# Kernel optimization log

Measured on AMD Instinct MI355X. Metric: run time of the kernel, lower is better.

## Reference

```python
import jax, jax.numpy as jnp
import numpy as np

EPS = 1e-5
SLOPE = 0.1


def _leaky(v):
    return jnp.where(v >= 0, v, SLOPE * v)


def _bn(v, gamma, beta):
    # v: (C, Q, k); training-mode batch norm over (Q, k) with biased variance
    m = v.mean(axis=(1, 2), keepdims=True)
    var = v.var(axis=(1, 2), keepdims=True)
    return (v - m) * jax.lax.rsqrt(var + EPS) * gamma[:, None, None] + beta[:, None, None]


def setup_inputs() -> dict:
    key = jax.random.key(0)
    ks = jax.random.split(key, 6)
    Q, S, K, F, O = 16384, 16384, 32, 64, 64
    q_points = jax.random.normal(ks[0], (Q, 3), dtype=jnp.float32)
    s_points = jax.random.normal(ks[1], (S, 3), dtype=jnp.float32)
    neighb_inds = jax.random.randint(ks[2], (Q, K), 0, S + 1)  # S is the padded zero row
    feat = jax.random.normal(ks[3], (S, F), dtype=jnp.float32)
    conv0_w = jax.random.normal(ks[4], (O, F), dtype=jnp.float32) * 0.1
    conv1_w = jax.random.normal(ks[5], (O * 3, O), dtype=jnp.float32) * 0.1
    return {
        "q_points": q_points,
        "s_points": s_points,
        "feat": feat,
        "neighb_inds": neighb_inds,
        "conv0_w": conv0_w,
        "gamma0": jnp.ones((O,), jnp.float32),
        "beta0": jnp.zeros((O,), jnp.float32),
        "conv1_w": conv1_w,
        "gamma1": jnp.ones((O,), jnp.float32),
        "beta1": jnp.zeros((O,), jnp.float32),
    }


def reference(q_points, s_points, feat, neighb_inds, conv0_w, gamma0, beta0, conv1_w, gamma1, beta1):
    Q, K = neighb_inds.shape
    n_supports = s_points.shape[0]
    out_c = conv1_w.shape[1]
    in_c = conv1_w.shape[0] // out_c  # = 3 for feat_mode='xyz'

    # pad with a zero row (index n_supports is the 'out of range' shadow point)
    s_pad = jnp.concatenate([s_points, jnp.zeros((1, s_points.shape[1]), s_points.dtype)], 0)
    f_pad = jnp.concatenate([feat, jnp.zeros((1, feat.shape[1]), feat.dtype)], 0)

    # relative xyz feature; zero out shadow neighbors
    x = s_pad[neighb_inds] - q_points[:, None, :]          # (Q, K, 3)
    mask = (neighb_inds == n_supports)[..., None]
    x = jnp.where(mask, jnp.zeros((), x.dtype), x)

    y = f_pad[neighb_inds]                                  # (Q, K, F)

    # kernel generation: conv0 (1x1) -> BN -> LeakyReLU -> conv1 (1x1)
    h = jnp.einsum('of,qkf->oqk', conv0_w, y)               # (O, Q, K)
    h = _leaky(_bn(h, gamma0, beta0))
    ker = jnp.einsum('co,oqk->qkc', conv1_w, h)             # (Q, K, O*in_c)
    ker = ker.reshape(Q, K, out_c, in_c)                    # (Q, K, O, 3)

    # per-edge matmul against relative xyz, then BN -> LeakyReLU -> max over k
    z = jnp.einsum('qkoi,qki->oqk', ker, x)                 # (O, Q, K)
    z = _leaky(_bn(z, gamma1, beta1))
    z = z.max(axis=2)                                       # (O, Q)
    return z.T                                              # (Q, O)
```

## Files before the change

### kernel.cpp

```cpp
#include <hip/hip_runtime.h>
#include <hip/hip_bf16.h>

typedef __attribute__((ext_vector_type(8))) short bf16x8;
typedef __attribute__((ext_vector_type(4))) short bf16x4;
typedef __attribute__((ext_vector_type(4))) float f32x4;

#define LEAKY(v) ((v) >= 0.f ? (v) : 0.1f * (v))

constexpr int Q = 16384, S = 16384, KNN = 32, F = 64, O = 64;
constexpr int NEDGE = Q * KNN;
constexpr int QB = 8;
constexpr int EB = 256;
constexpr int GD = Q / QB;
constexpr int GH = 128;
constexpr int FP = 72;
constexpr float EPSV = 1e-5f;

constexpr size_t CNT_OFF  = 0;
constexpr size_t P0_OFF   = 65536;
constexpr size_t ST0_OFF  = P0_OFF + (size_t)GH * 128 * 4;
constexpr size_t ZMIN_OFF = ST0_OFF + 512;
constexpr size_t P1_OFF   = ZMIN_OFF + (size_t)Q * O * 4;
constexpr size_t ST1_OFF  = P1_OFF + (size_t)GD * 128 * 4;
constexpr size_t W0F_OFF  = ST1_OFF + 512;
constexpr size_t W1F_OFF  = W0F_OFF + 8192;

__device__ __forceinline__ short f2bf(float f) {
  __hip_bfloat16 h = __float2bfloat16(f);
  short r; __builtin_memcpy(&r, &h, 2); return r;
}

__global__ void k_hist(const int* __restrict__ inds, int* __restrict__ cnt) {
  int i = blockIdx.x * blockDim.x + threadIdx.x;
  int stride = gridDim.x * blockDim.x;
  for (; i < NEDGE; i += stride) {
    int idx = inds[i];
    if (idx < S) atomicAdd(&cnt[idx], 1);
  }
}

__global__ void k_prep(const float* __restrict__ w0g, const float* __restrict__ w1g,
                       short* __restrict__ w0f, short* __restrict__ w1f) {
  const int t = blockIdx.x * 256 + threadIdx.x;
  const int fa = t >> 6, ln = t & 63;
  const int l4 = ln >> 4, l15 = ln & 15;
  if (fa < 8) {
    const int mt = fa >> 1, kk = fa & 1;
    const int o = 16 * mt + l15, f = 32 * kk + 8 * l4;
    const float* src = w0g + o * 64 + f;
    bf16x8 pk;
#pragma unroll
    for (int j = 0; j < 8; ++j) pk[j] = f2bf(src[j]);
    *(bf16x8*)&w0f[t * 8] = pk;
  } else {
    const int fb = fa - 8;
    const int nt = fb >> 1, kk = fb & 1;
    const int i = nt >> 2, b = nt & 3;
    const int o = 16 * b + l15, op = 32 * kk + 8 * l4;
    const float* src = w1g + (o * 3 + i) * 64 + op;
    bf16x8 pk;
#pragma unroll
    for (int j = 0; j < 8; ++j) pk[j] = f2bf(src[j]);
    *(bf16x8*)&w1f[(fb * 64 + ln) * 8] = pk;
  }
}

__global__ void k_hsq(const float* __restrict__ feat, const int* __restrict__ cnt,
                      const short* __restrict__ w0f, float* __restrict__ p0) {
  __shared__ float sred[4][2][64];
  const int t = threadIdx.x, blk = blockIdx.x;
  const int wv = t >> 6, ln = t & 63, l4 = ln >> 4, l15 = ln & 15;

  const bf16x8* w0v = (const bf16x8*)w0f;
  bf16x8 w0a[8];
#pragma unroll
  for (int fa = 0; fa < 8; ++fa) w0a[fa] = w0v[fa * 64 + ln];

  float hs[4][4], hq[4][4];
#pragma unroll
  for (int mt = 0; mt < 4; ++mt)
#pragma unroll
    for (int r = 0; r < 4; ++r) { hs[mt][r] = 0.f; hq[mt][r] = 0.f; }

#pragma unroll
  for (int tile = 0; tile < 2; ++tile) {
    const int s0 = blk * 128 + (wv * 2 + tile) * 16;
    const float wc = (float)cnt[s0 + l15];
    const float4* fr = (const float4*)(feat + (size_t)(s0 + l15) * 64);
    float4 a = fr[2 * l4], b = fr[2 * l4 + 1];
    float4 c = fr[8 + 2 * l4], d = fr[9 + 2 * l4];
    bf16x8 y0, y1;
    y0[0] = f2bf(a.x); y0[1] = f2bf(a.y); y0[2] = f2bf(a.z); y0[3] = f2bf(a.w);
    y0[4] = f2bf(b.x); y0[5] = f2bf(b.y); y0[6] = f2bf(b.z); y0[7] = f2bf(b.w);
    y1[0] = f2bf(c.x); y1[1] = f2bf(c.y); y1[2] = f2bf(c.z); y1[3] = f2bf(c.w);
    y1[4] = f2bf(d.x); y1[5] = f2bf(d.y); y1[6] = f2bf(d.z); y1[7] = f2bf(d.w);
#pragma unroll
    for (int mt = 0; mt < 4; ++mt) {
      f32x4 acc = {0.f, 0.f, 0.f, 0.f};
      acc = __builtin_amdgcn_mfma_f32_16x16x32_bf16(w0a[2 * mt], y0, acc, 0, 0, 0);
      acc = __builtin_amdgcn_mfma_f32_16x16x32_bf16(w0a[2 * mt + 1], y1, acc, 0, 0, 0);
#pragma unroll
      for (int r = 0; r < 4; ++r) {
        float h = acc[r];
        hs[mt][r] += wc * h;
        hq[mt][r] += wc * h * h;
      }
    }
  }
#pragma unroll
  for (int mt = 0; mt < 4; ++mt)
#pragma unroll
    for (int r = 0; r < 4; ++r) {
      float s = hs[mt][r], q = hq[mt][r];
#pragma unroll
      for (int d = 1; d < 16; d <<= 1) { s += __shfl_xor(s, d); q += __shfl_xor(q, d); }
      hs[mt][r] = s; hq[mt][r] = q;
    }
  if (l15 == 0) {
#pragma unroll
    for (int mt = 0; mt < 4; ++mt)
#pragma unroll
      for (int r = 0; r < 4; ++r) {
        const int o = 16 * mt + 4 * l4 + r;
        sred[wv][0][o] = hs[mt][r];
        sred[wv][1][o] = hq[mt][r];
      }
  }
  __syncthreads();
  if (t < 128) {
    const int qq = t >> 6, o = t & 63;
    p0[(size_t)blk * 128 + t] =
        sred[0][qq][o] + sred[1][qq][o] + sred[2][qq][o] + sred[3][qq][o];
  }
}

__global__ void k_stats0(const float* __restrict__ p0, const float* __restrict__ g0,
                         const float* __restrict__ b0, float* __restrict__ st0) {
  const int t = threadIdx.x;
  if (t < O) {
    float s = 0.f, q = 0.f;
    for (int b = 0; b < GH; ++b) {
      s += p0[(size_t)b * 128 + t];
      q += p0[(size_t)b * 128 + 64 + t];
    }
    const float invN = 1.f / (float)NEDGE;
    float mean = s * invN;
    float var = q * invN - mean * mean;
    float sc = g0[t] * rsqrtf(var + EPSV);
    st0[t] = sc;
    st0[O + t] = b0[t] - mean * sc;
  }
}

__launch_bounds__(256, 3)
__global__ void k_main(const float* __restrict__ qpts, const float* __restrict__ spts,
                       const float* __restrict__ feat, const int* __restrict__ inds,
                       const short* __restrict__ w0f, const short* __restrict__ w1f,
                       const float* __restrict__ st0,
                       float* __restrict__ zmax, float* __restrict__ zmin,
                       float* __restrict__ p1) {
  __shared__ __align__(16) short ybuf[EB * FP];
  __shared__ __align__(16) float xb[3 * EB];
  __shared__ float swred[4][128];

  const int t = threadIdx.x, blk = blockIdx.x;
  const int wv = t >> 6, ln = t & 63, l4 = ln >> 4, l15 = ln & 15;

  {
    const int e = t;
    const int idx = inds[(size_t)blk * EB + e];
    const int q = blk * QB + (e >> 5);
    float x0 = 0.f, x1 = 0.f, x2 = 0.f;
    if (idx < S) {
      x0 = spts[idx * 3 + 0] - qpts[q * 3 + 0];
      x1 = spts[idx * 3 + 1] - qpts[q * 3 + 1];
      x2 = spts[idx * 3 + 2] - qpts[q * 3 + 2];
      const float4* fr = (const float4*)(feat + (size_t)idx * F);
#pragma unroll
      for (int c = 0; c < 8; ++c) {
        float4 a = fr[2 * c], b = fr[2 * c + 1];
        bf16x8 pk;
        pk[0] = f2bf(a.x); pk[1] = f2bf(a.y); pk[2] = f2bf(a.z); pk[3] = f2bf(a.w);
        pk[4] = f2bf(b.x); pk[5] = f2bf(b.y); pk[6] = f2bf(b.z); pk[7] = f2bf(b.w);
        *(bf16x8*)&ybuf[e * FP + 8 * c] = pk;
      }
    } else {
      bf16x8 pk;
#pragma unroll
      for (int j = 0; j < 8; ++j) pk[j] = 0;
#pragma unroll
      for (int c = 0; c < 8; ++c) *(bf16x8*)&ybuf[e * FP + 8 * c] = pk;
    }
    xb[0 * EB + e] = x0; xb[1 * EB + e] = x1; xb[2 * EB + e] = x2;
  }

  float scr[4][4], shr[4][4];
#pragma unroll
  for (int mt = 0; mt < 4; ++mt)
#pragma unroll
    for (int r = 0; r < 4; ++r) {
      int o = 16 * mt + 4 * l4 + r;
      scr[mt][r] = st0[o]; shr[mt][r] = st0[O + o];
    }

  const bf16x8* w0v = (const bf16x8*)w0f;
  bf16x8 w0a[8];
#pragma unroll
  for (int fa = 0; fa < 8; ++fa) w0a[fa] = w0v[fa * 64 + ln];

  __syncthreads();

#pragma unroll
  for (int nt = 0; nt < 4; ++nt) {
    const int erow = wv * 64 + nt * 16 + l15;
    bf16x8 y0 = *(const bf16x8*)&ybuf[erow * FP + 8 * l4];
    bf16x8 y1 = *(const bf16x8*)&ybuf[erow * FP + 32 + 8 * l4];
#pragma unroll
    for (int mt = 0; mt < 4; ++mt) {
      f32x4 acc = {0.f, 0.f, 0.f, 0.f};
      acc = __builtin_amdgcn_mfma_f32_16x16x32_bf16(w0a[2 * mt], y0, acc, 0, 0, 0);
      acc = __builtin_amdgcn_mfma_f32_16x16x32_bf16(w0a[2 * mt + 1], y1, acc, 0, 0, 0);
      bf16x4 hv;
#pragma unroll
      for (int r = 0; r < 4; ++r) {
        float v = acc[r] * scr[mt][r] + shr[mt][r];
        v = LEAKY(v);
        hv[r] = f2bf(v);
      }
      *(bf16x4*)&ybuf[erow * FP + 16 * mt + 4 * l4] = hv;
    }
  }

  bf16x8 hA[4][2];
  f32x4 xv[4][3];
#pragma unroll
  for (int mt = 0; mt < 4; ++mt) {
    const int erow = wv * 64 + mt * 16 + l15;
    hA[mt][0] = *(const bf16x8*)&ybuf[erow * FP + 8 * l4];
    hA[mt][1] = *(const bf16x8*)&ybuf[erow * FP + 32 + 8 * l4];
    const int ex = wv * 64 + mt * 16 + 4 * l4;
#pragma unroll
    for (int i = 0; i < 3; ++i) xv[mt][i] = *(const f32x4*)&xb[i * EB + ex];
  }

  const bf16x8* w1v = (const bf16x8*)w1f;
  float zmx[2][4], zmn[2][4], zs[4], zq[4];
#pragma unroll
  for (int j = 0; j < 4; ++j) {
    zs[j] = 0.f; zq[j] = 0.f;
    zmx[0][j] = -3.4e38f; zmx[1][j] = -3.4e38f;
    zmn[0][j] = 3.4e38f;  zmn[1][j] = 3.4e38f;
  }

#pragma unroll
  for (int b = 0; b < 4; ++b) {
    bf16x8 w1b[6];
#pragma unroll
    for (int i = 0; i < 3; ++i)
#pragma unroll
      for (int kk = 0; kk < 2; ++kk)
        w1b[i * 2 + kk] = w1v[(((i * 4 + b) * 2) + kk) * 64 + ln];
#pragma unroll
    for (int mt = 0; mt < 4; ++mt) {
      f32x4 z4 = {0.f, 0.f, 0.f, 0.f};
#pragma unroll
      for (int i = 0; i < 3; ++i) {
        f32x4 acc = {0.f, 0.f, 0.f, 0.f};
        acc = __builtin_amdgcn_mfma_f32_16x16x32_bf16(hA[mt][0], w1b[2 * i], acc, 0, 0, 0);
        acc = __builtin_amdgcn_mfma_f32_16x16x32_bf16(hA[mt][1], w1b[2 * i + 1], acc, 0, 0, 0);
#pragma unroll
        for (int r = 0; r < 4; ++r) z4[r] += acc[r] * xv[mt][i][r];
      }
      const int qh = mt >> 1;
#pragma unroll
      for (int r = 0; r < 4; ++r) {
        float v = z4[r];
        zmx[qh][b] = fmaxf(zmx[qh][b], v);
        zmn[qh][b] = fminf(zmn[qh][b], v);
        zs[b] += v; zq[b] += v * v;
      }
    }
  }

#pragma unroll
  for (int qh = 0; qh < 2; ++qh)
#pragma unroll
    for (int b = 0; b < 4; ++b) {
      float m = zmx[qh][b];
      m = fmaxf(m, __shfl_xor(m, 16)); m = fmaxf(m, __shfl_xor(m, 32));
      zmx[qh][b] = m;
      float n = zmn[qh][b];
      n = fminf(n, __shfl_xor(n, 16)); n = fminf(n, __shfl_xor(n, 32));
      zmn[qh][b] = n;
    }
#pragma unroll
  for (int b = 0; b < 4; ++b) {
    float s = zs[b];  s += __shfl_xor(s, 16);  s += __shfl_xor(s, 32);  zs[b] = s;
    float sq = zq[b]; sq += __shfl_xor(sq, 16); sq += __shfl_xor(sq, 32); zq[b] = sq;
  }

  if (l4 == 0) {
#pragma unroll
    for (int qh = 0; qh < 2; ++qh) {
      const int q = blk * QB + wv * 2 + qh;
#pragma unroll
      for (int b = 0; b < 4; ++b) {
        zmax[(size_t)q * O + 16 * b + l15] = zmx[qh][b];
        zmin[(size_t)q * O + 16 * b + l15] = zmn[qh][b];
      }
    }
#pragma unroll
    for (int b = 0; b < 4; ++b) {
      swred[wv][16 * b + l15] = zs[b];
      swred[wv][64 + 16 * b + l15] = zq[b];
    }
  }
  __syncthreads();
  if (t < 128)
    p1[(size_t)blk * 128 + t] = swred[0][t] + swred[1][t] + swred[2][t] + swred[3][t];
}

__global__ void k_red1(const float* __restrict__ p1, const float* __restrict__ g1,
                       const float* __restrict__ b1, float* __restrict__ st1) {
  __shared__ float rs[256], rq[256];
  const int o = blockIdx.x, t = threadIdx.x;
  float s = 0.f, q = 0.f;
  for (int r = t; r < GD; r += 256) {
    s += p1[(size_t)r * 128 + o];
    q += p1[(size_t)r * 128 + 64 + o];
  }
  rs[t] = s; rq[t] = q;
  __syncthreads();
  for (int off = 128; off > 0; off >>= 1) {
    if (t < off) { rs[t] += rs[t + off]; rq[t] += rq[t + off]; }
    __syncthreads();
  }
  if (t == 0) {
    const float invN = 1.f / (float)NEDGE;
    float mean = rs[0] * invN;
    float var = rq[0] * invN - mean * mean;
    float sc = g1[o] * rsqrtf(var + EPSV);
    st1[o] = sc;
    st1[O + o] = b1[o] - mean * sc;
  }
}

__global__ void k_final(const float* __restrict__ st1, const float* __restrict__ zmin,
                        float* __restrict__ out) {
  int i = blockIdx.x * blockDim.x + threadIdx.x;
  if (i < Q * O) {
    int o = i & 63;
    float sc = st1[o], sh = st1[O + o];
    float base = (sc >= 0.f) ? out[i] : zmin[i];
    float v = base * sc + sh;
    out[i] = LEAKY(v);
  }
}

extern "C" void kernel_launch(void* const* d_in, const int* in_sizes, int n_in,
                              void* d_out, int out_size, void* d_ws, size_t ws_size,
                              hipStream_t stream) {
  const float* qpts = (const float*)d_in[0];
  const float* spts = (const float*)d_in[1];
  const float* feat = (const float*)d_in[2];
  const int*   inds = (const int*)d_in[3];
  const float* w0   = (const float*)d_in[4];
  const float* g0   = (const float*)d_in[5];
  const float* b0   = (const float*)d_in[6];
  const float* w1   = (const float*)d_in[7];
  const float* g1   = (const float*)d_in[8];
  const float* b1   = (const float*)d_in[9];
  float* out = (float*)d_out;

  char* ws = (char*)d_ws;
  int*   cnt  = (int*)(ws + CNT_OFF);
  float* p0   = (float*)(ws + P0_OFF);
  float* st0  = (float*)(ws + ST0_OFF);
  float* zmin = (float*)(ws + ZMIN_OFF);
  float* p1   = (float*)(ws + P1_OFF);
  float* st1  = (float*)(ws + ST1_OFF);
  short* w0f  = (short*)(ws + W0F_OFF);
  short* w1f  = (short*)(ws + W1F_OFF);

  hipMemsetAsync(cnt, 0, (size_t)S * sizeof(int), stream);
  k_prep<<<8, 256, 0, stream>>>(w0, w1, w0f, w1f);
  k_hist<<<512, 256, 0, stream>>>(inds, cnt);
  k_hsq<<<GH, 256, 0, stream>>>(feat, cnt, w0f, p0);
  k_stats0<<<1, 64, 0, stream>>>(p0, g0, b0, st0);
  k_main<<<GD, 256, 0, stream>>>(qpts, spts, feat, inds, w0f, w1f, st0, out, zmin, p1);
  k_red1<<<64, 256, 0, stream>>>(p1, g1, b1, st1);
  k_final<<<(Q * O) / 256, 256, 0, stream>>>(st1, zmin, out);
}
```

Before: 89.49 us.

## Fuse prep/hist and stats0 into neighbours, load features straight into MFMA registers

Merges weight packing with the index histogram into one launch and vectorises the histogram to int4 loads. The BN0 stats reduction moves into k_hsq through a last-block atomic counter. In k_main, gathered features go straight from global memory into MFMA operand registers instead of being staged through shared memory, the pre-MFMA barrier is removed, shared memory is reused for the reduction, and occupancy is raised to 4 blocks. These changes cut launch overhead, LDS traffic and register pressure, at the cost of per-lane gathers of 16-byte pieces of feature rows.

```diff
diff --git a/kernel.cpp b/kernel.cpp
--- a/kernel.cpp
+++ b/kernel.cpp
@@ -17,7 +17,8 @@
 constexpr float EPSV = 1e-5f;
 
 constexpr size_t CNT_OFF  = 0;
-constexpr size_t P0_OFF   = 65536;
+constexpr size_t CTR_OFF  = 65536;
+constexpr size_t P0_OFF   = 65600;
 constexpr size_t ST0_OFF  = P0_OFF + (size_t)GH * 128 * 4;
 constexpr size_t ZMIN_OFF = ST0_OFF + 512;
 constexpr size_t P1_OFF   = ZMIN_OFF + (size_t)Q * O * 4;
@@ -30,44 +31,48 @@
   short r; __builtin_memcpy(&r, &h, 2); return r;
 }
 
-__global__ void k_hist(const int* __restrict__ inds, int* __restrict__ cnt) {
-  int i = blockIdx.x * blockDim.x + threadIdx.x;
-  int stride = gridDim.x * blockDim.x;
-  for (; i < NEDGE; i += stride) {
-    int idx = inds[i];
-    if (idx < S) atomicAdd(&cnt[idx], 1);
-  }
-}
-
-__global__ void k_prep(const float* __restrict__ w0g, const float* __restrict__ w1g,
-                       short* __restrict__ w0f, short* __restrict__ w1f) {
-  const int t = blockIdx.x * 256 + threadIdx.x;
-  const int fa = t >> 6, ln = t & 63;
-  const int l4 = ln >> 4, l15 = ln & 15;
-  if (fa < 8) {
-    const int mt = fa >> 1, kk = fa & 1;
-    const int o = 16 * mt + l15, f = 32 * kk + 8 * l4;
-    const float* src = w0g + o * 64 + f;
-    bf16x8 pk;
-#pragma unroll
-    for (int j = 0; j < 8; ++j) pk[j] = f2bf(src[j]);
-    *(bf16x8*)&w0f[t * 8] = pk;
+__global__ void k_prep_hist(const float* __restrict__ w0g, const float* __restrict__ w1g,
+                            short* __restrict__ w0f, short* __restrict__ w1f,
+                            const int* __restrict__ inds, int* __restrict__ cnt) {
+  if (blockIdx.x < 8) {
+    const int t = blockIdx.x * 256 + threadIdx.x;
+    const int fa = t >> 6, ln = t & 63;
+    const int l4 = ln >> 4, l15 = ln & 15;
+    if (fa < 8) {
+      const int mt = fa >> 1, kk = fa & 1;
+      const int o = 16 * mt + l15, f = 32 * kk + 8 * l4;
+      const float* src = w0g + o * 64 + f;
+      bf16x8 pk;
+#pragma unroll
+      for (int j = 0; j < 8; ++j) pk[j] = f2bf(src[j]);
+      *(bf16x8*)&w0f[t * 8] = pk;
+    } else {
+      const int fb = fa - 8;
+      const int nt = fb >> 1, kk = fb & 1;
+      const int i = nt >> 2, b = nt & 3;
+      const int o = 16 * b + l15, op = 32 * kk + 8 * l4;
+      const float* src = w1g + (o * 3 + i) * 64 + op;
+      bf16x8 pk;
+#pragma unroll
+      for (int j = 0; j < 8; ++j) pk[j] = f2bf(src[j]);
+      *(bf16x8*)&w1f[(fb * 64 + ln) * 8] = pk;
+    }
   } else {
-    const int fb = fa - 8;
-    const int nt = fb >> 1, kk = fb & 1;
-    const int i = nt >> 2, b = nt & 3;
-    const int o = 16 * b + l15, op = 32 * kk + 8 * l4;
-    const float* src = w1g + (o * 3 + i) * 64 + op;
-    bf16x8 pk;
-#pragma unroll
-    for (int j = 0; j < 8; ++j) pk[j] = f2bf(src[j]);
-    *(bf16x8*)&w1f[(fb * 64 + ln) * 8] = pk;
+    const int i = (blockIdx.x - 8) * 256 + threadIdx.x;
+    const int4 v = ((const int4*)inds)[i];
+    if (v.x < S) atomicAdd(&cnt[v.x], 1);
+    if (v.y < S) atomicAdd(&cnt[v.y], 1);
+    if (v.z < S) atomicAdd(&cnt[v.z], 1);
+    if (v.w < S) atomicAdd(&cnt[v.w], 1);
   }
 }
 
 __global__ void k_hsq(const float* __restrict__ feat, const int* __restrict__ cnt,
-                      const short* __restrict__ w0f, float* __restrict__ p0) {
+                      const short* __restrict__ w0f, float* __restrict__ p0,
+                      int* __restrict__ ctr, const float* __restrict__ g0,
+                      const float* __restrict__ b0, float* __restrict__ st0) {
   __shared__ float sred[4][2][64];
+  __shared__ int isLast;
   const int t = threadIdx.x, blk = blockIdx.x;
   const int wv = t >> 6, ln = t & 63, l4 = ln >> 4, l15 = ln & 15;
 
@@ -132,66 +137,53 @@
     p0[(size_t)blk * 128 + t] =
         sred[0][qq][o] + sred[1][qq][o] + sred[2][qq][o] + sred[3][qq][o];
   }
-}
-
-__global__ void k_stats0(const float* __restrict__ p0, const float* __restrict__ g0,
-                         const float* __restrict__ b0, float* __restrict__ st0) {
-  const int t = threadIdx.x;
-  if (t < O) {
-    float s = 0.f, q = 0.f;
-    for (int b = 0; b < GH; ++b) {
-      s += p0[(size_t)b * 128 + t];
-      q += p0[(size_t)b * 128 + 64 + t];
-    }
-    const float invN = 1.f / (float)NEDGE;
-    float mean = s * invN;
-    float var = q * invN - mean * mean;
-    float sc = g0[t] * rsqrtf(var + EPSV);
-    st0[t] = sc;
-    st0[O + t] = b0[t] - mean * sc;
-  }
-}
-
-__launch_bounds__(256, 3)
+  __syncthreads();
+  __threadfence();
+  if (t == 0) isLast = (atomicAdd(&ctr[0], 1) == GH - 1);
+  __syncthreads();
+  if (isLast) {
+    __threadfence();
+    if (t < O) {
+      float s = 0.f, q = 0.f;
+      for (int b = 0; b < GH; ++b) {
+        s += p0[(size_t)b * 128 + t];
+        q += p0[(size_t)b * 128 + 64 + t];
+      }
+      const float invN = 1.f / (float)NEDGE;
+      float mean = s * invN;
+      float var = q * invN - mean * mean;
+      float sc = g0[t] * rsqrtf(var + EPSV);
+      st0[t] = sc;
+      st0[O + t] = b0[t] - mean * sc;
+    }
+  }
+}
+
+__launch_bounds__(256, 4)
 __global__ void k_main(const float* __restrict__ qpts, const float* __restrict__ spts,
                        const float* __restrict__ feat, const int* __restrict__ inds,
                        const short* __restrict__ w0f, const short* __restrict__ w1f,
                        const float* __restrict__ st0,
                        float* __restrict__ zmax, float* __restrict__ zmin,
                        float* __restrict__ p1) {
-  __shared__ __align__(16) short ybuf[EB * FP];
-  __shared__ __align__(16) float xb[3 * EB];
-  __shared__ float swred[4][128];
+  __shared__ __align__(16) short hbuf[EB * FP];
+  __shared__ __align__(16) float xs[3 * EB];
 
   const int t = threadIdx.x, blk = blockIdx.x;
   const int wv = t >> 6, ln = t & 63, l4 = ln >> 4, l15 = ln & 15;
+  const int ebase = blk * EB;
 
   {
     const int e = t;
-    const int idx = inds[(size_t)blk * EB + e];
+    const int idx = inds[ebase + e];
     const int q = blk * QB + (e >> 5);
     float x0 = 0.f, x1 = 0.f, x2 = 0.f;
     if (idx < S) {
       x0 = spts[idx * 3 + 0] - qpts[q * 3 + 0];
       x1 = spts[idx * 3 + 1] - qpts[q * 3 + 1];
       x2 = spts[idx * 3 + 2] - qpts[q * 3 + 2];
-      const float4* fr = (const float4*)(feat + (size_t)idx * F);
-#pragma unroll
-      for (int c = 0; c < 8; ++c) {
-        float4 a = fr[2 * c], b = fr[2 * c + 1];
-        bf16x8 pk;
-        pk[0] = f2bf(a.x); pk[1] = f2bf(a.y); pk[2] = f2bf(a.z); pk[3] = f2bf(a.w);
-        pk[4] = f2bf(b.x); pk[5] = f2bf(b.y); pk[6] = f2bf(b.z); pk[7] = f2bf(b.w);
-        *(bf16x8*)&ybuf[e * FP + 8 * c] = pk;
-      }
-    } else {
-      bf16x8 pk;
-#pragma unroll
-      for (int j = 0; j < 8; ++j) pk[j] = 0;
-#pragma unroll
-      for (int c = 0; c < 8; ++c) *(bf16x8*)&ybuf[e * FP + 8 * c] = pk;
-    }
-    xb[0 * EB + e] = x0; xb[1 * EB + e] = x1; xb[2 * EB + e] = x2;
+    }
+    xs[0 * EB + e] = x0; xs[1 * EB + e] = x1; xs[2 * EB + e] = x2;
   }
 
   float scr[4][4], shr[4][4];
@@ -208,13 +200,25 @@
 #pragma unroll
   for (int fa = 0; fa < 8; ++fa) w0a[fa] = w0v[fa * 64 + ln];
 
-  __syncthreads();
-
 #pragma unroll
   for (int nt = 0; nt < 4; ++nt) {
     const int erow = wv * 64 + nt * 16 + l15;
-    bf16x8 y0 = *(const bf16x8*)&ybuf[erow * FP + 8 * l4];
-    bf16x8 y1 = *(const bf16x8*)&ybuf[erow * FP + 32 + 8 * l4];
+    const int idx = inds[ebase + erow];
+    bf16x8 y0, y1;
+    if (idx < S) {
+      const float* fr = feat + (size_t)idx * F + 8 * l4;
+      f32x4 a = *(const f32x4*)(fr);
+      f32x4 b = *(const f32x4*)(fr + 4);
+      f32x4 c = *(const f32x4*)(fr + 32);
+      f32x4 d = *(const f32x4*)(fr + 36);
+      y0[0] = f2bf(a[0]); y0[1] = f2bf(a[1]); y0[2] = f2bf(a[2]); y0[3] = f2bf(a[3]);
+      y0[4] = f2bf(b[0]); y0[5] = f2bf(b[1]); y0[6] = f2bf(b[2]); y0[7] = f2bf(b[3]);
+      y1[0] = f2bf(c[0]); y1[1] = f2bf(c[1]); y1[2] = f2bf(c[2]); y1[3] = f2bf(c[3]);
+      y1[4] = f2bf(d[0]); y1[5] = f2bf(d[1]); y1[6] = f2bf(d[2]); y1[7] = f2bf(d[3]);
+    } else {
+#pragma unroll
+      for (int j = 0; j < 8; ++j) { y0[j] = 0; y1[j] = 0; }
+    }
 #pragma unroll
     for (int mt = 0; mt < 4; ++mt) {
       f32x4 acc = {0.f, 0.f, 0.f, 0.f};
@@ -227,20 +231,16 @@
         v = LEAKY(v);
         hv[r] = f2bf(v);
       }
-      *(bf16x4*)&ybuf[erow * FP + 16 * mt + 4 * l4] = hv;
+      *(bf16x4*)&hbuf[erow * FP + 16 * mt + 4 * l4] = hv;
     }
   }
 
   bf16x8 hA[4][2];
-  f32x4 xv[4][3];
 #pragma unroll
   for (int mt = 0; mt < 4; ++mt) {
     const int erow = wv * 64 + mt * 16 + l15;
-    hA[mt][0] = *(const bf16x8*)&ybuf[erow * FP + 8 * l4];
-    hA[mt][1] = *(const bf16x8*)&ybuf[erow * FP + 32 + 8 * l4];
-    const int ex = wv * 64 + mt * 16 + 4 * l4;
-#pragma unroll
-    for (int i = 0; i < 3; ++i) xv[mt][i] = *(const f32x4*)&xb[i * EB + ex];
+    hA[mt][0] = *(const bf16x8*)&hbuf[erow * FP + 8 * l4];
+    hA[mt][1] = *(const bf16x8*)&hbuf[erow * FP + 32 + 8 * l4];
   }
 
   const bf16x8* w1v = (const bf16x8*)w1f;
@@ -262,14 +262,16 @@
         w1b[i * 2 + kk] = w1v[(((i * 4 + b) * 2) + kk) * 64 + ln];
 #pragma unroll
     for (int mt = 0; mt < 4; ++mt) {
+      const int ex = wv * 64 + mt * 16 + 4 * l4;
       f32x4 z4 = {0.f, 0.f, 0.f, 0.f};
 #pragma unroll
       for (int i = 0; i < 3; ++i) {
         f32x4 acc = {0.f, 0.f, 0.f, 0.f};
         acc = __builtin_amdgcn_mfma_f32_16x16x32_bf16(hA[mt][0], w1b[2 * i], acc, 0, 0, 0);
         acc = __builtin_amdgcn_mfma_f32_16x16x32_bf16(hA[mt][1], w1b[2 * i + 1], acc, 0, 0, 0);
-#pragma unroll
-        for (int r = 0; r < 4; ++r) z4[r] += acc[r] * xv[mt][i][r];
+        const f32x4 xv = *(const f32x4*)&xs[i * EB + ex];
+#pragma unroll
+        for (int r = 0; r < 4; ++r) z4[r] += acc[r] * xv[r];
       }
       const int qh = mt >> 1;
 #pragma unroll
@@ -309,15 +311,19 @@
         zmin[(size_t)q * O + 16 * b + l15] = zmn[qh][b];
       }
     }
+  }
+
+  __syncthreads();
+  if (l4 == 0) {
 #pragma unroll
     for (int b = 0; b < 4; ++b) {
-      swred[wv][16 * b + l15] = zs[b];
-      swred[wv][64 + 16 * b + l15] = zq[b];
+      xs[wv * 128 + 16 * b + l15] = zs[b];
+      xs[wv * 128 + 64 + 16 * b + l15] = zq[b];
     }
   }
   __syncthreads();
   if (t < 128)
-    p1[(size_t)blk * 128 + t] = swred[0][t] + swred[1][t] + swred[2][t] + swred[3][t];
+    p1[(size_t)blk * 128 + t] = xs[t] + xs[128 + t] + xs[256 + t] + xs[384 + t];
 }
 
 __global__ void k_red1(const float* __restrict__ p1, const float* __restrict__ g1,
@@ -374,6 +380,7 @@
 
   char* ws = (char*)d_ws;
   int*   cnt  = (int*)(ws + CNT_OFF);
+  int*   ctr  = (int*)(ws + CTR_OFF);
   float* p0   = (float*)(ws + P0_OFF);
   float* st0  = (float*)(ws + ST0_OFF);
   float* zmin = (float*)(ws + ZMIN_OFF);
@@ -382,11 +389,9 @@
   short* w0f  = (short*)(ws + W0F_OFF);
   short* w1f  = (short*)(ws + W1F_OFF);
 
-  hipMemsetAsync(cnt, 0, (size_t)S * sizeof(int), stream);
-  k_prep<<<8, 256, 0, stream>>>(w0, w1, w0f, w1f);
-  k_hist<<<512, 256, 0, stream>>>(inds, cnt);
-  k_hsq<<<GH, 256, 0, stream>>>(feat, cnt, w0f, p0);
-  k_stats0<<<1, 64, 0, stream>>>(p0, g0, b0, st0);
+  hipMemsetAsync(ws, 0, CTR_OFF + 64, stream);
+  k_prep_hist<<<520, 256, 0, stream>>>(w0, w1, w0f, w1f, inds, cnt);
+  k_hsq<<<GH, 256, 0, stream>>>(feat, cnt, w0f, p0, ctr, g0, b0, st0);
   k_main<<<GD, 256, 0, stream>>>(qpts, spts, feat, inds, w0f, w1f, st0, out, zmin, p1);
   k_red1<<<64, 256, 0, stream>>>(p1, g1, b1, st1);
   k_final<<<(Q * O) / 256, 256, 0, stream>>>(st1, zmin, out);
```

Result: slower. 96.65 us (+8.0%).
